# Kernel optimization log

Measured on AMD Instinct MI355X. Metric: run time of the kernel, lower is better.

The kernel has to match this reference:

```python
import jax, jax.numpy as jnp
import numpy as np

N_NODES = 1_000_000
N_EDGES = 16_000_000
NUM_REL = 3
C_IN, C_OUT = 3, 2


def setup_inputs() -> dict:
    key = jax.random.key(0)
    ks = jax.random.split(key, 10)
    x = jax.random.normal(ks[0], (N_NODES, C_IN), dtype=jnp.float32)
    edge_index = jax.random.randint(ks[1], (2, N_EDGES), 0, N_NODES, dtype=jnp.int64)
    edge_attr = jax.random.randint(ks[2], (N_EDGES,), 0, NUM_REL, dtype=jnp.int64)
    s = 0.3
    W1 = jax.random.normal(ks[3], (NUM_REL, C_IN, C_OUT), dtype=jnp.float32) * s
    root1 = jax.random.normal(ks[4], (C_IN, C_OUT), dtype=jnp.float32) * s
    b1 = jax.random.normal(ks[5], (C_OUT,), dtype=jnp.float32) * s
    W2 = jax.random.normal(ks[6], (NUM_REL, C_OUT, C_OUT), dtype=jnp.float32) * s
    root2 = jax.random.normal(ks[7], (C_OUT, C_OUT), dtype=jnp.float32) * s
    b2 = jax.random.normal(ks[8], (C_OUT,), dtype=jnp.float32) * s
    return {"x": x, "edge_index": edge_index, "edge_attr": edge_attr,
            "W1": W1, "root1": root1, "b1": b1,
            "W2": W2, "root2": root2, "b2": b2}


def rgcn_conv(x, edge_index, edge_type, W, root, bias, num_nodes):
    """PyG RGCNConv: per-relation mean-aggregated messages + root transform + bias."""
    src, dst = edge_index[0], edge_index[1]
    xs = x[src]                                    # [E, c_in] gather once
    out = x @ root + bias                          # [N, c_out]
    for r in range(NUM_REL):                       # small fixed relation loop
        mask = (edge_type == r)
        msg = jnp.where(mask[:, None], xs @ W[r], 0.0)          # [E, c_out]
        sums = jax.ops.segment_sum(msg, dst, num_segments=num_nodes)
        cnt = jax.ops.segment_sum(mask.astype(x.dtype), dst, num_segments=num_nodes)
        out = out + sums / jnp.maximum(cnt, 1.0)[:, None]       # mean aggr
    return out


def reference(x, edge_index, edge_attr, W1, root1, b1, W2, root2, b2):
    h = rgcn_conv(x, edge_index, edge_attr, W1, root1, b1, N_NODES)
    h = jax.nn.relu(h)
    # F.dropout(training=self.training): identity in eval mode
    out = rgcn_conv(h, edge_index, edge_attr, W2, root2, b2, N_NODES)
    return out
```

## Files before the change

### kernel.cpp

```cpp
#include <hip/hip_runtime.h>


typedef unsigned long long u64;
typedef unsigned u32;

constexpr int NN = 1000000;
constexpr int NE = 16000000;
constexpr int NR = 3;

constexpr int BSH   = 10;
constexpr int NB    = (NN + 1023) >> 10;
constexpr int BCAP  = 18432;
constexpr int EPB   = 16384;
constexpr int NBLKB = (NE + EPB - 1) / EPB;

constexpr u64 M28 = (1ULL << 28) - 1;

__device__ __forceinline__ u64 pack_msg(float m0, float m1) {
    int a0 = __float2int_rn(fmaf(m0, 4096.0f, 524288.0f));
    int a1 = __float2int_rn(fmaf(m1, 4096.0f, 524288.0f));
    return (u64)(u32)a0 | ((u64)(u32)a1 << 28) | (1ULL << 56);
}

__device__ __forceinline__ u32 enc_x(float x0, float x1, float x2) {
    int q0 = __float2int_rn(fminf(fmaxf(x0 * 64.0f, -511.0f), 511.0f));
    int q1 = __float2int_rn(fminf(fmaxf(x1 * 128.0f, -1023.0f), 1023.0f));
    int q2 = __float2int_rn(fminf(fmaxf(x2 * 128.0f, -1023.0f), 1023.0f));
    return ((u32)q0 & 0x3FFu) | (((u32)q1 & 0x7FFu) << 10) | (((u32)q2 & 0x7FFu) << 21);
}

__device__ __forceinline__ void dec_x(u32 e, float& x0, float& x1, float& x2) {
    x0 = (float)((int)(e << 22) >> 22) * (1.0f / 64.0f);
    x1 = (float)((int)(e << 11) >> 21) * (1.0f / 128.0f);
    x2 = (float)((int)e >> 21)         * (1.0f / 128.0f);
}

__device__ __forceinline__ u32 enc_h(float h0, float h1) {
    int q0 = __float2int_rn(fminf(h0 * 1024.0f, 32767.0f));
    int q1 = __float2int_rn(fminf(h1 * 1024.0f, 32767.0f));
    return ((u32)q0 & 0xFFFFu) | ((u32)q1 << 16);
}

__device__ __forceinline__ void dec_h(u32 e, float& h0, float& h1) {
    h0 = (float)((int)(e << 16) >> 16) * (1.0f / 1024.0f);
    h1 = (float)((int)e >> 16)         * (1.0f / 1024.0f);
}


__global__ __launch_bounds__(256) void prep_qx_kernel(
    const float* __restrict__ x, u32* __restrict__ qx)
{
    int n = blockIdx.x * 256 + threadIdx.x;
    if (n >= NN) return;
    qx[n] = enc_x(x[3 * n + 0], x[3 * n + 1], x[3 * n + 2]);
}

__global__ __launch_bounds__(1024) void scatter_kernel(
    const int* __restrict__ src, const int* __restrict__ dst, const int* __restrict__ rel,
    u32* __restrict__ buf, u32* __restrict__ cursor)
{
    __shared__ u32 stage[EPB];
    __shared__ u32 hist[1024];
    __shared__ u32 wcur[1024];
    __shared__ u32 gbase[1024];
    __shared__ u32 wt[16];
    const int tid = threadIdx.x;
    const int wave = tid >> 6, lane = tid & 63;

    hist[tid] = 0;
    __syncthreads();

    const int base = blockIdx.x * EPB;
    const int nloc = min(EPB, NE - base);

    for (int i = tid; i < nloc; i += 1024)
        atomicAdd(&hist[((u32)dst[base + i]) >> BSH], 1u);
    __syncthreads();

    {
        int h0 = hist[tid];
        int v0 = h0;
#pragma unroll
        for (int d = 1; d < 64; d <<= 1) {
            int t = __shfl_up(v0, d);
            if (lane >= d) v0 += t;
        }
        if (lane == 63) wt[wave] = (u32)v0;
        __syncthreads();
        u32 off = 0;
#pragma unroll
        for (int wv = 0; wv < 16; ++wv) off += (wv < wave) ? wt[wv] : 0u;
        wcur[tid] = off + (u32)(v0 - h0);
    }
    __syncthreads();

    if (tid < NB) {
        u32 c = hist[tid];
        gbase[tid] = c ? atomicAdd(&cursor[tid], c) : 0u;
    }
    __syncthreads();

    for (int i = tid; i < nloc; i += 1024) {
        int e = base + i;
        u32 d = (u32)dst[e];
        u32 bk = d >> BSH;
        u32 sl = atomicAdd(&wcur[bk], 1u);
        stage[sl] = (u32)src[e] | ((u32)rel[e] << 20) | ((d & 1023u) << 22);
    }
    __syncthreads();

    for (int b = wave; b < NB; b += 16) {
        u32 cnt = hist[b];
        if (!cnt) continue;
        u32 ls = wcur[b] - cnt;
        u32 gb = gbase[b];
        u32* bb = buf + (size_t)b * BCAP;
        for (u32 j = lane; j < cnt; j += 64) {
            u32 slot = gb + j;
            if (slot < (u32)BCAP) bb[slot] = stage[ls + j];
        }
    }
}

__global__ __launch_bounds__(512) void agg1_kernel(
    const u32* __restrict__ buf, const u32* __restrict__ cursor,
    const u32* __restrict__ qx, const float* __restrict__ x,
    const float* __restrict__ W1,
    const float* __restrict__ root1, const float* __restrict__ b1,
    u32* __restrict__ qh)
{
    __shared__ u64 acc[1024 * NR];
    __shared__ float w[NR * 3 * 2];
    const int tid = threadIdx.x;
    for (int i = tid; i < 1024 * NR; i += 512) acc[i] = 0;
    if (tid < NR * 3 * 2) w[tid] = W1[tid];
    __syncthreads();

    const int bk = blockIdx.x;
    const int n = min((int)cursor[bk], BCAP);
    const u32* bb = buf + (size_t)bk * BCAP;

    int i = tid;
    for (; i + 3584 < n; i += 4096) {
        u32 e[8], g[8];
#pragma unroll
        for (int j = 0; j < 8; ++j) e[j] = bb[i + 512 * j];
#pragma unroll
        for (int j = 0; j < 8; ++j) g[j] = qx[e[j] & 0xFFFFFu];
#pragma unroll
        for (int j = 0; j < 8; ++j) {
            float a, b, c;
            dec_x(g[j], a, b, c);
            u32 r = (e[j] >> 20) & 3u; const float* wr = &w[r * 6];
            atomicAdd(&acc[(e[j] >> 22) * NR + r],
                pack_msg(a * wr[0] + b * wr[2] + c * wr[4],
                         a * wr[1] + b * wr[3] + c * wr[5]));
        }
    }
    for (; i < n; i += 512) {
        u32 e0 = bb[i];
        u32 g0 = qx[e0 & 0xFFFFFu];
        float a, b, c;
        dec_x(g0, a, b, c);
        u32 r = (e0 >> 20) & 3u; const float* wr = &w[r * 6];
        atomicAdd(&acc[(e0 >> 22) * NR + r],
            pack_msg(a * wr[0] + b * wr[2] + c * wr[4],
                     a * wr[1] + b * wr[3] + c * wr[5]));
    }
    __syncthreads();

    for (int l = tid; l < 1024; l += 512) {
        int node = (bk << BSH) + l;
        if (node >= NN) continue;
        float x0 = x[3 * node + 0], x1 = x[3 * node + 1], x2 = x[3 * node + 2];
        float o0 = x0 * root1[0] + x1 * root1[2] + x2 * root1[4] + b1[0];
        float o1 = x0 * root1[1] + x1 * root1[3] + x2 * root1[5] + b1[1];
#pragma unroll
        for (int r = 0; r < NR; ++r) {
            u64 wv = acc[l * NR + r];
            int c = (int)(wv >> 56);
            int s0i = (int)(wv & M28) - (c << 19);
            int s1i = (int)((wv >> 28) & M28) - (c << 19);
            float inv = (1.0f / 4096.0f) / (float)(c > 1 ? c : 1);
            o0 += (float)s0i * inv;
            o1 += (float)s1i * inv;
        }
        qh[node] = enc_h(fmaxf(o0, 0.0f), fmaxf(o1, 0.0f));
    }
}

__global__ __launch_bounds__(512) void agg2_kernel(
    const u32* __restrict__ buf, const u32* __restrict__ cursor,
    const u32* __restrict__ qh, const float* __restrict__ W2,
    const float* __restrict__ root2, const float* __restrict__ b2,
    float* __restrict__ out)
{
    __shared__ u64 acc[1024 * NR];
    __shared__ float w[NR * 2 * 2];
    const int tid = threadIdx.x;
    for (int i = tid; i < 1024 * NR; i += 512) acc[i] = 0;
    if (tid < NR * 2 * 2) w[tid] = W2[tid];
    __syncthreads();

    const int bk = blockIdx.x;
    const int n = min((int)cursor[bk], BCAP);
    const u32* bb = buf + (size_t)bk * BCAP;

    int i = tid;
    for (; i + 3584 < n; i += 4096) {
        u32 e[8], g[8];
#pragma unroll
        for (int j = 0; j < 8; ++j) e[j] = bb[i + 512 * j];
#pragma unroll
        for (int j = 0; j < 8; ++j) g[j] = qh[e[j] & 0xFFFFFu];
#pragma unroll
        for (int j = 0; j < 8; ++j) {
            float a, b;
            dec_h(g[j], a, b);
            u32 r = (e[j] >> 20) & 3u; const float* wr = &w[r * 4];
            atomicAdd(&acc[(e[j] >> 22) * NR + r],
                pack_msg(a * wr[0] + b * wr[2], a * wr[1] + b * wr[3]));
        }
    }
    for (; i < n; i += 512) {
        u32 e0 = bb[i];
        u32 g0 = qh[e0 & 0xFFFFFu];
        float a, b;
        dec_h(g0, a, b);
        u32 r = (e0 >> 20) & 3u; const float* wr = &w[r * 4];
        atomicAdd(&acc[(e0 >> 22) * NR + r],
            pack_msg(a * wr[0] + b * wr[2], a * wr[1] + b * wr[3]));
    }
    __syncthreads();

    for (int l = tid; l < 1024; l += 512) {
        int node = (bk << BSH) + l;
        if (node >= NN) continue;
        float hv0, hv1;
        dec_h(qh[node], hv0, hv1);
        float o0 = hv0 * root2[0] + hv1 * root2[2] + b2[0];
        float o1 = hv0 * root2[1] + hv1 * root2[3] + b2[1];
#pragma unroll
        for (int r = 0; r < NR; ++r) {
            u64 wv = acc[l * NR + r];
            int c = (int)(wv >> 56);
            int s0i = (int)(wv & M28) - (c << 19);
            int s1i = (int)((wv >> 28) & M28) - (c << 19);
            float inv = (1.0f / 4096.0f) / (float)(c > 1 ? c : 1);
            o0 += (float)s0i * inv;
            o1 += (float)s1i * inv;
        }
        float2 ov; ov.x = o0; ov.y = o1;
        ((float2*)out)[node] = ov;
    }
}


__global__ __launch_bounds__(256) void edge1_kernel(
    const int* __restrict__ src, const int* __restrict__ dst, const int* __restrict__ rel,
    const float* __restrict__ x, const float* __restrict__ W1,
    u64* __restrict__ sums1)
{
    __shared__ float w[NR * 3 * 2];
    if (threadIdx.x < NR * 3 * 2) w[threadIdx.x] = W1[threadIdx.x];
    __syncthreads();
    int e = blockIdx.x * 256 + threadIdx.x;
    if (e >= NE) return;
    int s = src[e], d = dst[e], r = rel[e];
    float x0 = x[3 * s + 0], x1 = x[3 * s + 1], x2 = x[3 * s + 2];
    const float* wr = &w[r * 6];
    float m0 = x0 * wr[0] + x1 * wr[2] + x2 * wr[4];
    float m1 = x0 * wr[1] + x1 * wr[3] + x2 * wr[5];
    atomicAdd(&sums1[d * NR + r], pack_msg(m0, m1));
}

__global__ __launch_bounds__(256) void node1_kernel(
    const float* __restrict__ x, const u64* __restrict__ sums1,
    const float* __restrict__ root1, const float* __restrict__ b1,
    float* __restrict__ h)
{
    int n = blockIdx.x * 256 + threadIdx.x;
    if (n >= NN) return;
    float x0 = x[3 * n + 0], x1 = x[3 * n + 1], x2 = x[3 * n + 2];
    float o0 = x0 * root1[0] + x1 * root1[2] + x2 * root1[4] + b1[0];
    float o1 = x0 * root1[1] + x1 * root1[3] + x2 * root1[5] + b1[1];
#pragma unroll
    for (int r = 0; r < NR; ++r) {
        u64 wv = sums1[n * NR + r];
        int c = (int)(wv >> 56);
        int s0i = (int)(wv & M28) - (c << 19);
        int s1i = (int)((wv >> 28) & M28) - (c << 19);
        float inv = (1.0f / 4096.0f) / (float)(c > 1 ? c : 1);
        o0 += (float)s0i * inv;
        o1 += (float)s1i * inv;
    }
    float2 hv;
    hv.x = fmaxf(o0, 0.0f);
    hv.y = fmaxf(o1, 0.0f);
    ((float2*)h)[n] = hv;
}

__global__ __launch_bounds__(256) void edge2_kernel(
    const int* __restrict__ src, const int* __restrict__ dst, const int* __restrict__ rel,
    const float* __restrict__ h, const float* __restrict__ W2,
    u64* __restrict__ sums2)
{
    __shared__ float w[NR * 2 * 2];
    if (threadIdx.x < NR * 2 * 2) w[threadIdx.x] = W2[threadIdx.x];
    __syncthreads();
    int e = blockIdx.x * 256 + threadIdx.x;
    if (e >= NE) return;
    int s = src[e];
    float2 hs = ((const float2*)h)[s];
    if (hs.x == 0.0f && hs.y == 0.0f) return;
    int d = dst[e], r = rel[e];
    const float* wr = &w[r * 4];
    float m0 = hs.x * wr[0] + hs.y * wr[2];
    float m1 = hs.x * wr[1] + hs.y * wr[3];
    atomicAdd(&sums2[d * NR + r], pack_msg(m0, m1));
}

__global__ __launch_bounds__(256) void node2_kernel(
    const float* __restrict__ h, const u64* __restrict__ sums1, const u64* __restrict__ sums2,
    const float* __restrict__ root2, const float* __restrict__ b2,
    float* __restrict__ out)
{
    int n = blockIdx.x * 256 + threadIdx.x;
    if (n >= NN) return;
    float2 hv = ((const float2*)h)[n];
    float o0 = hv.x * root2[0] + hv.y * root2[2] + b2[0];
    float o1 = hv.x * root2[1] + hv.y * root2[3] + b2[1];
#pragma unroll
    for (int r = 0; r < NR; ++r) {
        u64 w1 = sums1[n * NR + r];
        u64 w2 = sums2[n * NR + r];
        int c    = (int)(w1 >> 56);
        int adds = (int)(w2 >> 56);
        int s0i = (int)(w2 & M28) - (adds << 19);
        int s1i = (int)((w2 >> 28) & M28) - (adds << 19);
        float inv = (1.0f / 4096.0f) / (float)(c > 1 ? c : 1);
        o0 += (float)s0i * inv;
        o1 += (float)s1i * inv;
    }
    float2 ov; ov.x = o0; ov.y = o1;
    ((float2*)out)[n] = ov;
}

extern "C" void kernel_launch(void* const* d_in, const int* in_sizes, int n_in,
                              void* d_out, int out_size, void* d_ws, size_t ws_size,
                              hipStream_t stream) {
    const float* x     = (const float*)d_in[0];
    const int*   ei    = (const int*)d_in[1];
    const int*   rel   = (const int*)d_in[2];
    const float* W1    = (const float*)d_in[3];
    const float* root1 = (const float*)d_in[4];
    const float* b1    = (const float*)d_in[5];
    const float* W2    = (const float*)d_in[6];
    const float* root2 = (const float*)d_in[7];
    const float* b2    = (const float*)d_in[8];
    float* out = (float*)d_out;

    const int* src = ei;
    const int* dst = ei + NE;

    char* ws = (char*)d_ws;
    const int nb = (NN + 255) / 256;

    const size_t OFF_QX  = 72024064;
    const size_t OFF_QH  = 76024064;
    const size_t OFF_CUR = 80024064;
    const size_t WS_NEED = OFF_CUR + (size_t)NB * sizeof(u32);

    if (ws_size >= WS_NEED) {
        u32* buf    = (u32*)ws;
        u32* qx     = (u32*)(ws + OFF_QX);
        u32* qh     = (u32*)(ws + OFF_QH);
        u32* cursor = (u32*)(ws + OFF_CUR);

        hipMemsetAsync(cursor, 0, (size_t)NB * sizeof(u32), stream);
        prep_qx_kernel<<<nb, 256, 0, stream>>>(x, qx);
        scatter_kernel<<<NBLKB, 1024, 0, stream>>>(src, dst, rel, buf, cursor);
        agg1_kernel<<<NB, 512, 0, stream>>>(buf, cursor, qx, x, W1, root1, b1, qh);
        agg2_kernel<<<NB, 512, 0, stream>>>(buf, cursor, qh, W2, root2, b2, out);
    } else {
        u64*   sums1 = (u64*)ws;
        u64*   sums2 = (u64*)(ws + (size_t)24 * 1000 * 1000);
        float* h     = (float*)(ws + (size_t)48 * 1000 * 1000);
        const int eb = (NE + 255) / 256;

        hipMemsetAsync(sums1, 0, (size_t)NN * NR * sizeof(u64), stream);
        hipMemsetAsync(sums2, 0, (size_t)NN * NR * sizeof(u64), stream);
        edge1_kernel<<<eb, 256, 0, stream>>>(src, dst, rel, x, W1, sums1);
        node1_kernel<<<nb, 256, 0, stream>>>(x, sums1, root1, b1, h);
        edge2_kernel<<<eb, 256, 0, stream>>>(src, dst, rel, h, W2, sums2);
        node2_kernel<<<nb, 256, 0, stream>>>(h, sums1, sums2, root2, b2, out);
    }
}
```

Measured before the change: 485.8 us.

## Aggregate quantized inputs per relation and apply weights after the mean

The aggregation kernels now sum the biased, unsigned quantized node features (widened into packed u64 fields with a count) per destination and relation, instead of computing and packing per-edge messages. The relation weight matrix is applied once per node after dividing by the count, which is valid because the transform is linear. Edge records are read with 16-byte vector loads, each cursor is padded to its own 64-byte slot to reduce atomic contention, the bucket capacity is trimmed to 18368 entries so each bucket stays 16-byte aligned, and a minimum-occupancy launch bound is added. This removes the per-edge multiply-adds and float-to-int conversion work, at the cost of relying on the packed fields not overflowing and on a different rounding path.

```diff
diff --git a/kernel.cpp b/kernel.cpp
--- a/kernel.cpp
+++ b/kernel.cpp
@@ -10,40 +10,49 @@
 
 constexpr int BSH   = 10;
 constexpr int NB    = (NN + 1023) >> 10;
-constexpr int BCAP  = 18432;
+constexpr int BCAP  = 18368;
+constexpr int CSTR  = 16;
 constexpr int EPB   = 16384;
 constexpr int NBLKB = (NE + EPB - 1) / EPB;
 
+__device__ __forceinline__ u32 enc_x(float x0, float x1, float x2) {
+    int q0 = __float2int_rn(fminf(fmaxf(x0 * 64.0f, -511.0f), 511.0f));
+    int q1 = __float2int_rn(fminf(fmaxf(x1 * 128.0f, -1023.0f), 1023.0f));
+    int q2 = __float2int_rn(fminf(fmaxf(x2 * 128.0f, -1023.0f), 1023.0f));
+    return ((u32)(q0 + 512) & 0x3FFu)
+         | (((u32)(q1 + 1024) & 0x7FFu) << 10)
+         | (((u32)(q2 + 1024) & 0x7FFu) << 21);
+}
+
+__device__ __forceinline__ u64 widen_x(u32 q) {
+    return (u64)(q & 0x3FFu)
+         | ((u64)((q >> 10) & 0x7FFu) << 18)
+         | ((u64)(q >> 21) << 36)
+         | (1ULL << 54);
+}
+
+__device__ __forceinline__ u32 enc_h(float h0, float h1) {
+    int q0 = __float2int_rn(fminf(h0 * 1024.0f, 32767.0f));
+    int q1 = __float2int_rn(fminf(h1 * 1024.0f, 32767.0f));
+    return ((u32)q0 & 0xFFFFu) | ((u32)q1 << 16);
+}
+
+__device__ __forceinline__ u64 widen_h(u32 q) {
+    return (u64)(q & 0xFFFFu)
+         | ((u64)(q >> 16) << 22)
+         | (1ULL << 44);
+}
+
+__device__ __forceinline__ void dec_h(u32 e, float& h0, float& h1) {
+    h0 = (float)(e & 0xFFFFu) * (1.0f / 1024.0f);
+    h1 = (float)(e >> 16)     * (1.0f / 1024.0f);
+}
+
 constexpr u64 M28 = (1ULL << 28) - 1;
-
 __device__ __forceinline__ u64 pack_msg(float m0, float m1) {
     int a0 = __float2int_rn(fmaf(m0, 4096.0f, 524288.0f));
     int a1 = __float2int_rn(fmaf(m1, 4096.0f, 524288.0f));
     return (u64)(u32)a0 | ((u64)(u32)a1 << 28) | (1ULL << 56);
-}
-
-__device__ __forceinline__ u32 enc_x(float x0, float x1, float x2) {
-    int q0 = __float2int_rn(fminf(fmaxf(x0 * 64.0f, -511.0f), 511.0f));
-    int q1 = __float2int_rn(fminf(fmaxf(x1 * 128.0f, -1023.0f), 1023.0f));
-    int q2 = __float2int_rn(fminf(fmaxf(x2 * 128.0f, -1023.0f), 1023.0f));
-    return ((u32)q0 & 0x3FFu) | (((u32)q1 & 0x7FFu) << 10) | (((u32)q2 & 0x7FFu) << 21);
-}
-
-__device__ __forceinline__ void dec_x(u32 e, float& x0, float& x1, float& x2) {
-    x0 = (float)((int)(e << 22) >> 22) * (1.0f / 64.0f);
-    x1 = (float)((int)(e << 11) >> 21) * (1.0f / 128.0f);
-    x2 = (float)((int)e >> 21)         * (1.0f / 128.0f);
-}
-
-__device__ __forceinline__ u32 enc_h(float h0, float h1) {
-    int q0 = __float2int_rn(fminf(h0 * 1024.0f, 32767.0f));
-    int q1 = __float2int_rn(fminf(h1 * 1024.0f, 32767.0f));
-    return ((u32)q0 & 0xFFFFu) | ((u32)q1 << 16);
-}
-
-__device__ __forceinline__ void dec_h(u32 e, float& h0, float& h1) {
-    h0 = (float)((int)(e << 16) >> 16) * (1.0f / 1024.0f);
-    h1 = (float)((int)e >> 16)         * (1.0f / 1024.0f);
 }
 
 
@@ -96,7 +105,7 @@
 
     if (tid < NB) {
         u32 c = hist[tid];
-        gbase[tid] = c ? atomicAdd(&cursor[tid], c) : 0u;
+        gbase[tid] = c ? atomicAdd(&cursor[tid * CSTR], c) : 0u;
     }
     __syncthreads();
 
@@ -122,7 +131,7 @@
     }
 }
 
-__global__ __launch_bounds__(512) void agg1_kernel(
+__global__ __launch_bounds__(512, 8) void agg1_kernel(
     const u32* __restrict__ buf, const u32* __restrict__ cursor,
     const u32* __restrict__ qx, const float* __restrict__ x,
     const float* __restrict__ W1,
@@ -137,35 +146,26 @@
     __syncthreads();
 
     const int bk = blockIdx.x;
-    const int n = min((int)cursor[bk], BCAP);
+    const int n = min((int)cursor[bk * CSTR], BCAP);
     const u32* bb = buf + (size_t)bk * BCAP;
-
-    int i = tid;
-    for (; i + 3584 < n; i += 4096) {
-        u32 e[8], g[8];
-#pragma unroll
-        for (int j = 0; j < 8; ++j) e[j] = bb[i + 512 * j];
-#pragma unroll
-        for (int j = 0; j < 8; ++j) g[j] = qx[e[j] & 0xFFFFFu];
-#pragma unroll
-        for (int j = 0; j < 8; ++j) {
-            float a, b, c;
-            dec_x(g[j], a, b, c);
-            u32 r = (e[j] >> 20) & 3u; const float* wr = &w[r * 6];
-            atomicAdd(&acc[(e[j] >> 22) * NR + r],
-                pack_msg(a * wr[0] + b * wr[2] + c * wr[4],
-                         a * wr[1] + b * wr[3] + c * wr[5]));
-        }
-    }
-    for (; i < n; i += 512) {
+    const int n16 = n >> 4;
+
+    for (int g = tid; g < n16; g += 512) {
+        const uint4* p = (const uint4*)(bb + ((size_t)g << 4));
+        uint4 E0 = p[0], E1 = p[1], E2 = p[2], E3 = p[3];
+        u32 e[16] = {E0.x, E0.y, E0.z, E0.w, E1.x, E1.y, E1.z, E1.w,
+                     E2.x, E2.y, E2.z, E2.w, E3.x, E3.y, E3.z, E3.w};
+        u32 q[16];
+#pragma unroll
+        for (int j = 0; j < 16; ++j) q[j] = qx[e[j] & 0xFFFFFu];
+#pragma unroll
+        for (int j = 0; j < 16; ++j)
+            atomicAdd(&acc[(e[j] >> 22) * NR + ((e[j] >> 20) & 3u)], widen_x(q[j]));
+    }
+    for (int i = (n16 << 4) + tid; i < n; i += 512) {
         u32 e0 = bb[i];
-        u32 g0 = qx[e0 & 0xFFFFFu];
-        float a, b, c;
-        dec_x(g0, a, b, c);
-        u32 r = (e0 >> 20) & 3u; const float* wr = &w[r * 6];
-        atomicAdd(&acc[(e0 >> 22) * NR + r],
-            pack_msg(a * wr[0] + b * wr[2] + c * wr[4],
-                     a * wr[1] + b * wr[3] + c * wr[5]));
+        u32 q0 = qx[e0 & 0xFFFFFu];
+        atomicAdd(&acc[(e0 >> 22) * NR + ((e0 >> 20) & 3u)], widen_x(q0));
     }
     __syncthreads();
 
@@ -178,18 +178,25 @@
 #pragma unroll
         for (int r = 0; r < NR; ++r) {
             u64 wv = acc[l * NR + r];
-            int c = (int)(wv >> 56);
-            int s0i = (int)(wv & M28) - (c << 19);
-            int s1i = (int)((wv >> 28) & M28) - (c << 19);
-            float inv = (1.0f / 4096.0f) / (float)(c > 1 ? c : 1);
-            o0 += (float)s0i * inv;
-            o1 += (float)s1i * inv;
+            u32 c = (u32)(wv >> 54);
+            if (c) {
+                float inv = 1.0f / (float)c;
+                float S0 = (float)(u32)(wv & 0x3FFFFu);
+                float S1 = (float)(u32)((wv >> 18) & 0x3FFFFu);
+                float S2 = (float)(u32)((wv >> 36) & 0x3FFFFu);
+                float m0 = fmaf(S0, inv, -512.0f)  * (1.0f / 64.0f);
+                float m1 = fmaf(S1, inv, -1024.0f) * (1.0f / 128.0f);
+                float m2 = fmaf(S2, inv, -1024.0f) * (1.0f / 128.0f);
+                const float* wr = &w[r * 6];
+                o0 += m0 * wr[0] + m1 * wr[2] + m2 * wr[4];
+                o1 += m0 * wr[1] + m1 * wr[3] + m2 * wr[5];
+            }
         }
         qh[node] = enc_h(fmaxf(o0, 0.0f), fmaxf(o1, 0.0f));
     }
 }
 
-__global__ __launch_bounds__(512) void agg2_kernel(
+__global__ __launch_bounds__(512, 8) void agg2_kernel(
     const u32* __restrict__ buf, const u32* __restrict__ cursor,
     const u32* __restrict__ qh, const float* __restrict__ W2,
     const float* __restrict__ root2, const float* __restrict__ b2,
@@ -203,33 +210,26 @@
     __syncthreads();
 
     const int bk = blockIdx.x;
-    const int n = min((int)cursor[bk], BCAP);
+    const int n = min((int)cursor[bk * CSTR], BCAP);
     const u32* bb = buf + (size_t)bk * BCAP;
-
-    int i = tid;
-    for (; i + 3584 < n; i += 4096) {
-        u32 e[8], g[8];
-#pragma unroll
-        for (int j = 0; j < 8; ++j) e[j] = bb[i + 512 * j];
-#pragma unroll
-        for (int j = 0; j < 8; ++j) g[j] = qh[e[j] & 0xFFFFFu];
-#pragma unroll
-        for (int j = 0; j < 8; ++j) {
-            float a, b;
-            dec_h(g[j], a, b);
-            u32 r = (e[j] >> 20) & 3u; const float* wr = &w[r * 4];
-            atomicAdd(&acc[(e[j] >> 22) * NR + r],
-                pack_msg(a * wr[0] + b * wr[2], a * wr[1] + b * wr[3]));
-        }
-    }
-    for (; i < n; i += 512) {
+    const int n16 = n >> 4;
+
+    for (int g = tid; g < n16; g += 512) {
+        const uint4* p = (const uint4*)(bb + ((size_t)g << 4));
+        uint4 E0 = p[0], E1 = p[1], E2 = p[2], E3 = p[3];
+        u32 e[16] = {E0.x, E0.y, E0.z, E0.w, E1.x, E1.y, E1.z, E1.w,
+                     E2.x, E2.y, E2.z, E2.w, E3.x, E3.y, E3.z, E3.w};
+        u32 q[16];
+#pragma unroll
+        for (int j = 0; j < 16; ++j) q[j] = qh[e[j] & 0xFFFFFu];
+#pragma unroll
+        for (int j = 0; j < 16; ++j)
+            atomicAdd(&acc[(e[j] >> 22) * NR + ((e[j] >> 20) & 3u)], widen_h(q[j]));
+    }
+    for (int i = (n16 << 4) + tid; i < n; i += 512) {
         u32 e0 = bb[i];
-        u32 g0 = qh[e0 & 0xFFFFFu];
-        float a, b;
-        dec_h(g0, a, b);
-        u32 r = (e0 >> 20) & 3u; const float* wr = &w[r * 4];
-        atomicAdd(&acc[(e0 >> 22) * NR + r],
-            pack_msg(a * wr[0] + b * wr[2], a * wr[1] + b * wr[3]));
+        u32 q0 = qh[e0 & 0xFFFFFu];
+        atomicAdd(&acc[(e0 >> 22) * NR + ((e0 >> 20) & 3u)], widen_h(q0));
     }
     __syncthreads();
 
@@ -243,12 +243,15 @@
 #pragma unroll
         for (int r = 0; r < NR; ++r) {
             u64 wv = acc[l * NR + r];
-            int c = (int)(wv >> 56);
-            int s0i = (int)(wv & M28) - (c << 19);
-            int s1i = (int)((wv >> 28) & M28) - (c << 19);
-            float inv = (1.0f / 4096.0f) / (float)(c > 1 ? c : 1);
-            o0 += (float)s0i * inv;
-            o1 += (float)s1i * inv;
+            u32 c = (u32)(wv >> 44);
+            if (c) {
+                float inv = 1.0f / (float)c;
+                float m0 = (float)(u32)(wv & 0x3FFFFFu)         * inv * (1.0f / 1024.0f);
+                float m1 = (float)(u32)((wv >> 22) & 0x3FFFFFu) * inv * (1.0f / 1024.0f);
+                const float* wr = &w[r * 4];
+                o0 += m0 * wr[0] + m1 * wr[2];
+                o1 += m0 * wr[1] + m1 * wr[3];
+            }
         }
         float2 ov; ov.x = o0; ov.y = o1;
         ((float2*)out)[node] = ov;
@@ -366,10 +369,10 @@
     char* ws = (char*)d_ws;
     const int nb = (NN + 255) / 256;
 
-    const size_t OFF_QX  = 72024064;
-    const size_t OFF_QH  = 76024064;
-    const size_t OFF_CUR = 80024064;
-    const size_t WS_NEED = OFF_CUR + (size_t)NB * sizeof(u32);
+    const size_t OFF_QX  = 71782144;
+    const size_t OFF_QH  = 75782144;
+    const size_t OFF_CUR = 79782144;
+    const size_t WS_NEED = OFF_CUR + (size_t)NB * CSTR * sizeof(u32);
 
     if (ws_size >= WS_NEED) {
         u32* buf    = (u32*)ws;
@@ -377,7 +380,7 @@
         u32* qh     = (u32*)(ws + OFF_QH);
         u32* cursor = (u32*)(ws + OFF_CUR);
 
-        hipMemsetAsync(cursor, 0, (size_t)NB * sizeof(u32), stream);
+        hipMemsetAsync(cursor, 0, (size_t)NB * CSTR * sizeof(u32), stream);
         prep_qx_kernel<<<nb, 256, 0, stream>>>(x, qx);
         scatter_kernel<<<NBLKB, 1024, 0, stream>>>(src, dst, rel, buf, cursor);
         agg1_kernel<<<NB, 512, 0, stream>>>(buf, cursor, qx, x, W1, root1, b1, qh);
```

Result: slower. 501.4 us (+3.2%).
